# Optimization experiments

Measured on AMD Instinct MI355X. Metric: run time of the kernel, lower is better.

The kernel has to match this reference:

```python
import jax, jax.numpy as jnp
import numpy as np

H = 8  # num_heads

def layer_norm(x, g, b, eps=1e-5):
    mu = x.mean(-1, keepdims=True)
    var = ((x - mu) ** 2).mean(-1, keepdims=True)
    return (x - mu) / jnp.sqrt(var + eps) * g + b

def setup_inputs() -> dict:
    key = jax.random.key(0)
    ks = jax.random.split(key, 8)
    T, B, E, F = 64, 32, 512, 2048
    std = 0.02
    return {
        "x": jax.random.normal(ks[0], (T, B, E), jnp.float32),
        "relation": jax.random.normal(ks[1], (T, T, B, E), jnp.float32),
        "in_w": jax.random.normal(ks[2], (3 * E, E), jnp.float32) * std,
        "in_b": jnp.zeros((3 * E,), jnp.float32),
        "rel_w": jax.random.normal(ks[3], (E, 2 * E), jnp.float32) * std,
        "rel_b": jnp.zeros((2 * E,), jnp.float32),
        "out_w": jax.random.normal(ks[4], (E, E), jnp.float32) * std,
        "out_b": jnp.zeros((E,), jnp.float32),
        "fc1_w": jax.random.normal(ks[5], (E, F), jnp.float32) * std,
        "fc1_b": jnp.zeros((F,), jnp.float32),
        "fc2_w": jax.random.normal(ks[6], (F, E), jnp.float32) * std,
        "fc2_b": jnp.zeros((E,), jnp.float32),
        "ln1_g": jnp.ones((E,), jnp.float32),
        "ln1_b": jnp.zeros((E,), jnp.float32),
        "ln2_g": jnp.ones((E,), jnp.float32),
        "ln2_b": jnp.zeros((E,), jnp.float32),
    }

def reference(x, relation, in_w, in_b, rel_w, rel_b, out_w, out_b,
              fc1_w, fc1_b, fc2_w, fc2_b, ln1_g, ln1_b, ln2_g, ln2_b):
    T, B, E = x.shape
    Dh = E // H
    scaling = Dh ** -0.5
    # qkv projection (F.linear with weight [3E, E])
    qkv = x @ in_w.T + in_b                      # (T, B, 3E)
    q, k, v = jnp.split(qkv, 3, axis=-1)
    q = q.reshape(T, B * H, Dh)
    k = k.reshape(T, B * H, Dh)
    v = v.reshape(T, B * H, Dh)
    # relation bias: Conv1D(2E, E) -> ra, rb, view+transpose(0,1) as in torch
    r = relation @ rel_w + rel_b                 # (T, T, B, 2E)
    ra, rb = jnp.split(r, 2, axis=-1)
    ra = jnp.swapaxes(ra.reshape(T, T, B * H, Dh), 0, 1)
    rb = jnp.swapaxes(rb.reshape(T, T, B * H, Dh), 0, 1)
    # (q + ra) scaled, elementwise-reduce against (k + rb), extra 1/sqrt(Dh)
    q2 = (q[:, None] + ra) * scaling             # (T, T, BH, Dh)
    k2 = k[None, :] + rb                         # (T, T, BH, Dh)
    w = jnp.einsum('ijbn,ijbn->ijb', q2, k2) * scaling  # (T, T, BH)
    w = jax.nn.softmax(w, axis=1)                # softmax over src dim
    attn = jnp.einsum('ijb,jbn->bin', w, v)      # (BH, T, Dh)
    attn = jnp.swapaxes(attn, 0, 1).reshape(T, B, E)
    attn = attn @ out_w + out_b
    h = layer_norm(x + attn, ln1_g, ln1_b)
    f = jax.nn.relu(h @ fc1_w + fc1_b) @ fc2_w + fc2_b
    return layer_norm(h + f, ln2_g, ln2_b)
```

## Files before the change

kernel.cpp:

```cpp
#include <hip/hip_runtime.h>


typedef __bf16 bf16;
typedef __attribute__((ext_vector_type(8))) __bf16 bf16x8;
typedef __attribute__((ext_vector_type(4))) __bf16 bf16x4;
typedef __attribute__((ext_vector_type(4))) float f32x4;
typedef __attribute__((ext_vector_type(8))) short s16x8;


__device__ inline void fl_decode(int d, int NT, int& k, int& n) {
  int frag = d >> 9; int lane = (d >> 3) & 63; int j = d & 7;
  int kt = frag / NT, nt = frag - kt * NT;
  k = kt * 32 + ((lane >> 4) << 3) + j;
  n = nt * 16 + (lane & 15);
}

__global__ void prep_kernel(const float* __restrict__ x,
                            const float* __restrict__ in_w,
                            const float* __restrict__ rel_w,
                            const float* __restrict__ out_w,
                            const float* __restrict__ fc1_w,
                            const float* __restrict__ fc2_w,
                            bf16* __restrict__ x_b,
                            bf16* __restrict__ inw_fl,
                            bf16* __restrict__ relw_fl,
                            bf16* __restrict__ outw_fl,
                            bf16* __restrict__ fc1w_fl,
                            bf16* __restrict__ fc2w_fl) {
  int tid = blockIdx.x * 256 + threadIdx.x;
  int k, n;
  if (tid < 1048576) { x_b[tid] = (bf16)x[tid]; return; }
  tid -= 1048576;
  if (tid < 786432) {
    fl_decode(tid, 96, k, n);
    inw_fl[tid] = (bf16)in_w[n * 512 + k];
    return;
  }
  tid -= 786432;
  if (tid < 524288) {
    fl_decode(tid, 64, k, n);
    relw_fl[tid] = (bf16)rel_w[k * 1024 + n];
    return;
  }
  tid -= 524288;
  if (tid < 262144) {
    fl_decode(tid, 32, k, n);
    outw_fl[tid] = (bf16)out_w[k * 512 + n];
    return;
  }
  tid -= 262144;
  if (tid < 1048576) {
    fl_decode(tid, 128, k, n);
    fc1w_fl[tid] = (bf16)fc1_w[k * 2048 + n];
    return;
  }
  tid -= 1048576;
  if (tid < 1048576) {
    fl_decode(tid, 32, k, n);
    fc2w_fl[tid] = (bf16)fc2_w[k * 512 + n];
  }
}

template <bool RELU, bool WF32, bool WBF16>
__global__ __launch_bounds__(256, 2) void gemm_bf16(
    const bf16* __restrict__ A, const bf16* __restrict__ Bfl,
    const float* __restrict__ bias, float* __restrict__ Cf,
    bf16* __restrict__ Cb, int M, int N, int K) {
  __shared__ bf16 lA[4096];
  __shared__ bf16 lB[4096];
  const int tid = threadIdx.x;
  const int l = tid & 63;
  const int wv = tid >> 6;
  const int wm = wv >> 1, wn = wv & 1;
  const int m0 = blockIdx.x * 128, n0 = blockIdx.y * 128;
  const int NT = N >> 4;
  const int nb0 = n0 >> 4;
  const int KT = K >> 5;

  f32x4 acc[4][4];
#pragma unroll
  for (int i = 0; i < 4; i++)
#pragma unroll
    for (int j = 0; j < 4; j++) acc[i][j] = (f32x4)0.f;

  const int c = tid >> 5;
  const int lp0 = (tid & 31) * 2;

  for (int kt = 0; kt < KT; ++kt) {
#pragma unroll
    for (int u = 0; u < 2; ++u) {
      int lp = lp0 + u;
      int row = c * 16 + (lp & 15);
      int kof = (lp >> 4) << 3;
      s16x8 va = *(const s16x8*)(A + (long)(m0 + row) * K + kt * 32 + kof);
      *(s16x8*)(&lA[c * 512 + lp * 8]) = va;
    }
    {
      const s16x8* src = (const s16x8*)(Bfl + (long)(kt * NT + nb0) * 512);
      s16x8* dst = (s16x8*)lB;
      dst[tid] = src[tid];
      dst[tid + 256] = src[tid + 256];
    }
    __syncthreads();
    bf16x8 af[4], bfr[4];
#pragma unroll
    for (int mt = 0; mt < 4; mt++)
      af[mt] = *(const bf16x8*)(&lA[(wm * 4 + mt) * 512 + l * 8]);
#pragma unroll
    for (int nt = 0; nt < 4; nt++)
      bfr[nt] = *(const bf16x8*)(&lB[(wn * 4 + nt) * 512 + l * 8]);
#pragma unroll
    for (int mt = 0; mt < 4; mt++)
#pragma unroll
      for (int nt = 0; nt < 4; nt++)
        acc[mt][nt] = __builtin_amdgcn_mfma_f32_16x16x32_bf16(af[mt], bfr[nt],
                                                              acc[mt][nt], 0, 0, 0);
    __syncthreads();
  }
#pragma unroll
  for (int nt = 0; nt < 4; nt++) {
    int n = n0 + wn * 64 + nt * 16 + (l & 15);
    float bv = bias[n];
#pragma unroll
    for (int mt = 0; mt < 4; mt++) {
#pragma unroll
      for (int j = 0; j < 4; j++) {
        int row = m0 + wm * 64 + mt * 16 + ((l >> 4) << 2) + j;
        float v = acc[mt][nt][j] + bv;
        if (RELU) v = fmaxf(v, 0.f);
        if (WF32) Cf[(long)row * N + n] = v;
        if (WBF16) Cb[(long)row * N + n] = (bf16)v;
      }
    }
  }
}

__global__ __launch_bounds__(512, 2) void relw_kernel(
    const float* __restrict__ rel, const bf16* __restrict__ relw_fl,
    const float* __restrict__ rel_b, const float* __restrict__ qkv,
    float* __restrict__ wT) {
  __shared__ bf16 lA[2][2048];
  const int tid = threadIdx.x;
  const int l = tid & 63;
  const int h = tid >> 6;
  const int t1 = blockIdx.x >> 5;
  const int r2 = blockIdx.x & 31;
  const long row0 = ((long)t1 * 64 + r2 * 2) * 32;

  f32x4 acc[4][8];
#pragma unroll
  for (int i = 0; i < 4; i++)
#pragma unroll
    for (int j = 0; j < 8; j++) acc[i][j] = (f32x4)0.f;

  const int sr = tid >> 3;
  const int sg = tid & 7;
  const int smt = sr >> 4;
  const int slane = ((sg >> 1) << 4) + (sr & 15);
  const int sdst = smt * 512 + slane * 8 + (sg & 1) * 4;
  const float* srcbase = rel + (row0 + sr) * 512 + sg * 4;

  f32x4 stg = *(const f32x4*)(srcbase);
  for (int kt = 0; kt < 16; ++kt) {
    const int buf = kt & 1;
    bf16x4 cv;
#pragma unroll
    for (int u = 0; u < 4; ++u) cv[u] = (bf16)stg[u];
    *(bf16x4*)(&lA[buf][sdst]) = cv;
    f32x4 stg_next = stg;
    if (kt < 15) stg_next = *(const f32x4*)(srcbase + (kt + 1) * 32);
    __syncthreads();

    bf16x8 af[4];
#pragma unroll
    for (int mt = 0; mt < 4; mt++)
      af[mt] = *(const bf16x8*)(&lA[buf][mt * 512 + l * 8]);
    const bf16* bbase = relw_fl + ((long)kt * 64 + h * 4) * 512 + l * 8;
    bf16x8 bfr[8];
#pragma unroll
    for (int nt = 0; nt < 4; nt++) {
      bfr[nt] = *(const bf16x8*)(bbase + nt * 512);
      bfr[4 + nt] = *(const bf16x8*)(bbase + 16384 + nt * 512);
    }
#pragma unroll
    for (int mt = 0; mt < 4; mt++)
#pragma unroll
      for (int ns = 0; ns < 8; ns++)
        acc[mt][ns] = __builtin_amdgcn_mfma_f32_16x16x32_bf16(af[mt], bfr[ns],
                                                              acc[mt][ns], 0, 0, 0);
    stg = stg_next;
  }

  const int dhb = h * 64;
#pragma unroll
  for (int mt = 0; mt < 4; mt++) {
    float psum[4] = {0.f, 0.f, 0.f, 0.f};
#pragma unroll
    for (int nt = 0; nt < 4; nt++) {
      const int dh = nt * 16 + (l & 15);
      const float ba = rel_b[dhb + dh];
      const float bb2 = rel_b[512 + dhb + dh];
#pragma unroll
      for (int j = 0; j < 4; j++) {
        int rl = mt * 16 + ((l >> 4) << 2) + j;
        int b = rl & 31;
        int t2 = r2 * 2 + (rl >> 5);
        float qv = qkv[(long)(t2 * 32 + b) * 1536 + dhb + dh];
        float kv = qkv[(long)(t1 * 32 + b) * 1536 + 512 + dhb + dh];
        psum[j] += (qv + acc[mt][nt][j] + ba) * (kv + acc[mt][nt + 4][j] + bb2);
      }
    }
#pragma unroll
    for (int j = 0; j < 4; j++) {
      float v = psum[j];
      v += __shfl_xor(v, 1);
      v += __shfl_xor(v, 2);
      v += __shfl_xor(v, 4);
      v += __shfl_xor(v, 8);
      if ((l & 15) == 0) {
        int rl = mt * 16 + ((l >> 4) << 2) + j;
        int b = rl & 31;
        int i = r2 * 2 + (rl >> 5);
        wT[(long)(i * 256 + b * 8 + h) * 64 + t1] = v * 0.015625f;
      }
    }
  }
}

__global__ __launch_bounds__(256) void attn_kernel(const float* __restrict__ wT,
                                                   const float* __restrict__ qkv,
                                                   bf16* __restrict__ attn_b) {
  const int l = threadIdx.x & 63;
  const int g = blockIdx.x * 4 + (threadIdx.x >> 6);
  const int bh = g & 255;
  const int i = g >> 8;
  const int b = bh >> 3, h = bh & 7;
  float wv = wT[(long)g * 64 + l];
  float m = wv;
#pragma unroll
  for (int s = 1; s < 64; s <<= 1) m = fmaxf(m, __shfl_xor(m, s));
  float e = __expf(wv - m);
  float ssum = e;
#pragma unroll
  for (int s = 1; s < 64; s <<= 1) ssum += __shfl_xor(ssum, s);
  float p = e / ssum;
  float acc = 0.f;
  const float* vbase = qkv + 1024 + (long)b * 1536 + h * 64 + l;
#pragma unroll 8
  for (int j = 0; j < 64; ++j) {
    float pj = __shfl(p, j);
    acc = fmaf(pj, vbase[(long)j * 49152], acc);
  }
  attn_b[(long)(i * 32 + b) * 512 + h * 64 + l] = (bf16)acc;
}

template <bool WB>
__global__ __launch_bounds__(256) void ln_kernel(const float* __restrict__ a,
                                                 const float* __restrict__ res,
                                                 const float* __restrict__ g,
                                                 const float* __restrict__ bb,
                                                 float* __restrict__ of,
                                                 bf16* __restrict__ ob) {
  const int l = threadIdx.x & 63;
  const int row = blockIdx.x * 4 + (threadIdx.x >> 6);
  const float* pa = a + (long)row * 512;
  const float* pr = res + (long)row * 512;
  float xv[8];
  float s = 0.f, sq = 0.f;
#pragma unroll
  for (int u = 0; u < 8; ++u) {
    xv[u] = pa[u * 64 + l] + pr[u * 64 + l];
    s += xv[u];
    sq += xv[u] * xv[u];
  }
#pragma unroll
  for (int st = 1; st < 64; st <<= 1) {
    s += __shfl_xor(s, st);
    sq += __shfl_xor(sq, st);
  }
  float mean = s * (1.f / 512.f);
  float var = sq * (1.f / 512.f) - mean * mean;
  float rstd = rsqrtf(var + 1e-5f);
#pragma unroll
  for (int u = 0; u < 8; ++u) {
    int e = u * 64 + l;
    float v = (xv[u] - mean) * rstd * g[e] + bb[e];
    of[(long)row * 512 + e] = v;
    if (WB) ob[(long)row * 512 + e] = (bf16)v;
  }
}

extern "C" void kernel_launch(void* const* d_in, const int* in_sizes, int n_in,
                              void* d_out, int out_size, void* d_ws, size_t ws_size,
                              hipStream_t stream) {
  const float* x     = (const float*)d_in[0];
  const float* rel   = (const float*)d_in[1];
  const float* in_w  = (const float*)d_in[2];
  const float* in_b  = (const float*)d_in[3];
  const float* rel_w = (const float*)d_in[4];
  const float* rel_b = (const float*)d_in[5];
  const float* out_w = (const float*)d_in[6];
  const float* out_b = (const float*)d_in[7];
  const float* fc1_w = (const float*)d_in[8];
  const float* fc1_b = (const float*)d_in[9];
  const float* fc2_w = (const float*)d_in[10];
  const float* fc2_b = (const float*)d_in[11];
  const float* ln1_g = (const float*)d_in[12];
  const float* ln1_b = (const float*)d_in[13];
  const float* ln2_g = (const float*)d_in[14];
  const float* ln2_b = (const float*)d_in[15];

  char* ws = (char*)d_ws;
  float* qkv   = (float*)(ws + 0);
  bf16* x_b    = (bf16*)(ws + 12582912);
  bf16* inw    = (bf16*)(ws + 14680064);
  bf16* relwB  = (bf16*)(ws + 16252928);
  bf16* outwB  = (bf16*)(ws + 17301504);
  bf16* fc1wB  = (bf16*)(ws + 17825792);
  bf16* fc2wB  = (bf16*)(ws + 19922944);
  float* wT    = (float*)(ws + 22020096);
  bf16* attn   = (bf16*)(ws + 26214400);
  float* opre  = (float*)(ws + 28311552);
  float* hf    = (float*)(ws + 32505856);
  bf16* hb     = (bf16*)(ws + 36700160);
  bf16* fb     = (bf16*)(ws + 38797312);
  float* f2o   = (float*)(ws + 47185920);

  prep_kernel<<<18432, 256, 0, stream>>>(x, in_w, rel_w, out_w, fc1_w, fc2_w,
                                         x_b, inw, relwB, outwB, fc1wB, fc2wB);
  gemm_bf16<false, true, false><<<dim3(16, 12), 256, 0, stream>>>(
      x_b, inw, in_b, qkv, nullptr, 2048, 1536, 512);
  relw_kernel<<<2048, 512, 0, stream>>>(rel, relwB, rel_b, qkv, wT);
  attn_kernel<<<4096, 256, 0, stream>>>(wT, qkv, attn);
  gemm_bf16<false, true, false><<<dim3(16, 4), 256, 0, stream>>>(
      attn, outwB, out_b, opre, nullptr, 2048, 512, 512);
  ln_kernel<true><<<512, 256, 0, stream>>>(opre, x, ln1_g, ln1_b, hf, hb);
  gemm_bf16<true, false, true><<<dim3(16, 16), 256, 0, stream>>>(
      hb, fc1wB, fc1_b, nullptr, fb, 2048, 2048, 512);
  gemm_bf16<false, true, false><<<dim3(16, 4), 256, 0, stream>>>(
      fb, fc2wB, fc2_b, f2o, nullptr, 2048, 512, 2048);
  ln_kernel<false><<<512, 256, 0, stream>>>(f2o, hf, ln2_g, ln2_b, (float*)d_out,
                                            nullptr);
}
```

Before: 679.7 us.

## Vectorize weight prep, pipeline GEMMs and relation kernel, restructure attention

Weight conversion now uses vectorized float4 loads with one thread per 8 or 16 elements. The GEMM is templated on tile shape, uses direct global-to-LDS loads with double buffering, and launches smaller tiles for the narrow GEMMs so more blocks run. The relation kernel double-buffers its B-fragment register loads and prefetches activation data two steps ahead. Attention now processes one (b,h) per block, staging V and the probabilities in LDS to cut redundant strided global reads. These changes add LDS usage and register pressure, which may lower occupancy.

```diff
diff --git a/kernel.cpp b/kernel.cpp
--- a/kernel.cpp
+++ b/kernel.cpp
@@ -5,14 +5,34 @@
 typedef __attribute__((ext_vector_type(8))) __bf16 bf16x8;
 typedef __attribute__((ext_vector_type(4))) __bf16 bf16x4;
 typedef __attribute__((ext_vector_type(4))) float f32x4;
-typedef __attribute__((ext_vector_type(8))) short s16x8;
-
-
-__device__ inline void fl_decode(int d, int NT, int& k, int& n) {
-  int frag = d >> 9; int lane = (d >> 3) & 63; int j = d & 7;
+
+__device__ __forceinline__ void gl_lds16(const bf16* g, bf16* l) {
+  __builtin_amdgcn_global_load_lds((const __attribute__((address_space(1))) void*)g,
+                                   (__attribute__((address_space(3))) void*)l, 16, 0, 0);
+}
+
+__device__ __forceinline__ void block_sync_lds() {
+  asm volatile("s_waitcnt lgkmcnt(0)" ::: "memory");
+  __builtin_amdgcn_s_barrier();
+  asm volatile("" ::: "memory");
+}
+
+
+template <int NSRC, int NT>
+__device__ __forceinline__ void convkn(int t, const float* __restrict__ W,
+                                       bf16* __restrict__ dst) {
+  int frag = t >> 5, r = t & 31;
+  int lh = r >> 3, j = r & 7;
   int kt = frag / NT, nt = frag - kt * NT;
-  k = kt * 32 + ((lane >> 4) << 3) + j;
-  n = nt * 16 + (lane & 15);
+  int k = kt * 32 + lh * 8 + j;
+  const float* src = W + (long)k * NSRC + nt * 16;
+  f32x4 v0 = ((const f32x4*)src)[0], v1 = ((const f32x4*)src)[1];
+  f32x4 v2 = ((const f32x4*)src)[2], v3 = ((const f32x4*)src)[3];
+  bf16* d = dst + frag * 512 + lh * 128 + j;
+  d[0] = (bf16)v0[0];  d[8] = (bf16)v0[1];  d[16] = (bf16)v0[2];  d[24] = (bf16)v0[3];
+  d[32] = (bf16)v1[0]; d[40] = (bf16)v1[1]; d[48] = (bf16)v1[2];  d[56] = (bf16)v1[3];
+  d[64] = (bf16)v2[0]; d[72] = (bf16)v2[1]; d[80] = (bf16)v2[2];  d[88] = (bf16)v2[3];
+  d[96] = (bf16)v3[0]; d[104] = (bf16)v3[1]; d[112] = (bf16)v3[2]; d[120] = (bf16)v3[3];
 }
 
 __global__ void prep_kernel(const float* __restrict__ x,
@@ -27,105 +47,111 @@
                             bf16* __restrict__ outw_fl,
                             bf16* __restrict__ fc1w_fl,
                             bf16* __restrict__ fc2w_fl) {
-  int tid = blockIdx.x * 256 + threadIdx.x;
-  int k, n;
-  if (tid < 1048576) { x_b[tid] = (bf16)x[tid]; return; }
-  tid -= 1048576;
-  if (tid < 786432) {
-    fl_decode(tid, 96, k, n);
-    inw_fl[tid] = (bf16)in_w[n * 512 + k];
+  int t = blockIdx.x * 256 + threadIdx.x;
+  if (t < 131072) {
+    int d0 = t * 8;
+    f32x4 a = *(const f32x4*)(x + d0), b = *(const f32x4*)(x + d0 + 4);
+    bf16x8 r;
+    r[0] = (bf16)a[0]; r[1] = (bf16)a[1]; r[2] = (bf16)a[2]; r[3] = (bf16)a[3];
+    r[4] = (bf16)b[0]; r[5] = (bf16)b[1]; r[6] = (bf16)b[2]; r[7] = (bf16)b[3];
+    *(bf16x8*)(x_b + d0) = r;
     return;
   }
-  tid -= 786432;
-  if (tid < 524288) {
-    fl_decode(tid, 64, k, n);
-    relw_fl[tid] = (bf16)rel_w[k * 1024 + n];
+  t -= 131072;
+  if (t < 98304) {
+    int d0 = t * 8;
+    int frag = d0 >> 9, l = t & 63;
+    int kt = frag / 96, nt = frag - kt * 96;
+    const float* src = in_w + (long)(nt * 16 + (l & 15)) * 512 + kt * 32 + ((l >> 4) << 3);
+    f32x4 a = *(const f32x4*)src, b = *(const f32x4*)(src + 4);
+    bf16x8 r;
+    r[0] = (bf16)a[0]; r[1] = (bf16)a[1]; r[2] = (bf16)a[2]; r[3] = (bf16)a[3];
+    r[4] = (bf16)b[0]; r[5] = (bf16)b[1]; r[6] = (bf16)b[2]; r[7] = (bf16)b[3];
+    *(bf16x8*)(inw_fl + d0) = r;
     return;
   }
-  tid -= 524288;
-  if (tid < 262144) {
-    fl_decode(tid, 32, k, n);
-    outw_fl[tid] = (bf16)out_w[k * 512 + n];
-    return;
-  }
-  tid -= 262144;
-  if (tid < 1048576) {
-    fl_decode(tid, 128, k, n);
-    fc1w_fl[tid] = (bf16)fc1_w[k * 2048 + n];
-    return;
-  }
-  tid -= 1048576;
-  if (tid < 1048576) {
-    fl_decode(tid, 32, k, n);
-    fc2w_fl[tid] = (bf16)fc2_w[k * 512 + n];
-  }
-}
-
-template <bool RELU, bool WF32, bool WBF16>
+  t -= 98304;
+  if (t < 32768) { convkn<1024, 64>(t, rel_w, relw_fl); return; }
+  t -= 32768;
+  if (t < 16384) { convkn<512, 32>(t, out_w, outw_fl); return; }
+  t -= 16384;
+  if (t < 65536) { convkn<2048, 128>(t, fc1_w, fc1w_fl); return; }
+  t -= 65536;
+  if (t < 65536) { convkn<512, 32>(t, fc2_w, fc2w_fl); }
+}
+
+template <int WM, int WN, int MT, int NT, bool RELU, bool WF32, bool WBF16>
 __global__ __launch_bounds__(256, 2) void gemm_bf16(
     const bf16* __restrict__ A, const bf16* __restrict__ Bfl,
     const float* __restrict__ bias, float* __restrict__ Cf,
     bf16* __restrict__ Cb, int M, int N, int K) {
-  __shared__ bf16 lA[4096];
-  __shared__ bf16 lB[4096];
-  const int tid = threadIdx.x;
-  const int l = tid & 63;
-  const int wv = tid >> 6;
-  const int wm = wv >> 1, wn = wv & 1;
-  const int m0 = blockIdx.x * 128, n0 = blockIdx.y * 128;
-  const int NT = N >> 4;
-  const int nb0 = n0 >> 4;
-  const int KT = K >> 5;
-
-  f32x4 acc[4][4];
-#pragma unroll
-  for (int i = 0; i < 4; i++)
-#pragma unroll
-    for (int j = 0; j < 4; j++) acc[i][j] = (f32x4)0.f;
-
-  const int c = tid >> 5;
-  const int lp0 = (tid & 31) * 2;
+  constexpr int AFR = WM * MT;
+  constexpr int BFR = WN * NT;
+  constexpr int NA = AFR / 4, NB = BFR / 4;
+  __shared__ __align__(16) bf16 lA[2][AFR * 512];
+  __shared__ __align__(16) bf16 lB[2][BFR * 512];
+  const int tid = threadIdx.x, l = tid & 63, wv = tid >> 6;
+  const int wm = wv / WN, wn = wv % WN;
+  const int m0 = blockIdx.x * (AFR * 16), n0 = blockIdx.y * (BFR * 16);
+  const int NTfr = N >> 4, nb0 = n0 >> 4, KT = K >> 5;
+
+  f32x4 acc[MT][NT];
+#pragma unroll
+  for (int i = 0; i < MT; i++)
+#pragma unroll
+    for (int j = 0; j < NT; j++) acc[i][j] = (f32x4)0.f;
+
+  const bf16* pA[NA];
+#pragma unroll
+  for (int i = 0; i < NA; ++i) {
+    int f = wv + i * 4;
+    pA[i] = A + (long)(m0 + f * 16 + (l & 15)) * K + ((l >> 4) << 3);
+  }
+  const bf16* pB[NB];
+#pragma unroll
+  for (int i = 0; i < NB; ++i) {
+    int f = wv + i * 4;
+    pB[i] = Bfl + (long)(nb0 + f) * 512 + l * 8;
+  }
+#pragma unroll
+  for (int i = 0; i < NA; ++i) gl_lds16(pA[i], &lA[0][(wv + i * 4) * 512]);
+#pragma unroll
+  for (int i = 0; i < NB; ++i) gl_lds16(pB[i], &lB[0][(wv + i * 4) * 512]);
 
   for (int kt = 0; kt < KT; ++kt) {
-#pragma unroll
-    for (int u = 0; u < 2; ++u) {
-      int lp = lp0 + u;
-      int row = c * 16 + (lp & 15);
-      int kof = (lp >> 4) << 3;
-      s16x8 va = *(const s16x8*)(A + (long)(m0 + row) * K + kt * 32 + kof);
-      *(s16x8*)(&lA[c * 512 + lp * 8]) = va;
+    const int buf = kt & 1;
+    __syncthreads();
+    if (kt + 1 < KT) {
+#pragma unroll
+      for (int i = 0; i < NA; ++i)
+        gl_lds16(pA[i] + (kt + 1) * 32, &lA[buf ^ 1][(wv + i * 4) * 512]);
+#pragma unroll
+      for (int i = 0; i < NB; ++i)
+        gl_lds16(pB[i] + (long)(kt + 1) * NTfr * 512, &lB[buf ^ 1][(wv + i * 4) * 512]);
     }
-    {
-      const s16x8* src = (const s16x8*)(Bfl + (long)(kt * NT + nb0) * 512);
-      s16x8* dst = (s16x8*)lB;
-      dst[tid] = src[tid];
-      dst[tid + 256] = src[tid + 256];
-    }
-    __syncthreads();
-    bf16x8 af[4], bfr[4];
-#pragma unroll
-    for (int mt = 0; mt < 4; mt++)
-      af[mt] = *(const bf16x8*)(&lA[(wm * 4 + mt) * 512 + l * 8]);
-#pragma unroll
-    for (int nt = 0; nt < 4; nt++)
-      bfr[nt] = *(const bf16x8*)(&lB[(wn * 4 + nt) * 512 + l * 8]);
-#pragma unroll
-    for (int mt = 0; mt < 4; mt++)
-#pragma unroll
-      for (int nt = 0; nt < 4; nt++)
+    bf16x8 af[MT], bfr[NT];
+#pragma unroll
+    for (int mt = 0; mt < MT; ++mt)
+      af[mt] = *(const bf16x8*)(&lA[buf][(wm * MT + mt) * 512 + l * 8]);
+#pragma unroll
+    for (int nt = 0; nt < NT; ++nt)
+      bfr[nt] = *(const bf16x8*)(&lB[buf][(wn * NT + nt) * 512 + l * 8]);
+#pragma unroll
+    for (int mt = 0; mt < MT; ++mt)
+#pragma unroll
+      for (int nt = 0; nt < NT; ++nt)
         acc[mt][nt] = __builtin_amdgcn_mfma_f32_16x16x32_bf16(af[mt], bfr[nt],
                                                               acc[mt][nt], 0, 0, 0);
-    __syncthreads();
-  }
-#pragma unroll
-  for (int nt = 0; nt < 4; nt++) {
-    int n = n0 + wn * 64 + nt * 16 + (l & 15);
+  }
+#pragma unroll
+  for (int nt = 0; nt < NT; nt++) {
+    int n = n0 + (wn * NT + nt) * 16 + (l & 15);
     float bv = bias[n];
 #pragma unroll
-    for (int mt = 0; mt < 4; mt++) {
+    for (int mt = 0; mt < MT; mt++) {
 #pragma unroll
       for (int j = 0; j < 4; j++) {
-        int row = m0 + wm * 64 + mt * 16 + ((l >> 4) << 2) + j;
+        int row = m0 + (wm * MT + mt) * 16 + ((l >> 4) << 2) + j;
         float v = acc[mt][nt][j] + bv;
         if (RELU) v = fmaxf(v, 0.f);
         if (WF32) Cf[(long)row * N + n] = v;
@@ -135,11 +161,33 @@
   }
 }
 
+#define RELW_STEP(kt_, buf_, BC, BN, STG_W, STG_P)                               \
+  {                                                                              \
+    bf16x4 cv;                                                                   \
+    cv[0] = (bf16)STG_W[0]; cv[1] = (bf16)STG_W[1];                              \
+    cv[2] = (bf16)STG_W[2]; cv[3] = (bf16)STG_W[3];                              \
+    *(bf16x4*)(&lA[buf_][adst]) = cv;                                            \
+    block_sync_lds();                                                            \
+    if ((kt_) + 2 < 16) STG_P = *(const f32x4*)(asrc + ((kt_) + 2) * 32);        \
+    if ((kt_) + 1 < 16) {                                                        \
+      _Pragma("unroll") for (int f = 0; f < 8; ++f)                              \
+          BN[f] = *(const bf16x8*)(relw_fl + (long)((kt_) + 1) * 32768 + boff0 + \
+                                   (((f >> 2) * 32 + (f & 3)) << 9));            \
+    }                                                                            \
+    bf16x8 af[4];                                                                \
+    _Pragma("unroll") for (int mt = 0; mt < 4; mt++)                             \
+        af[mt] = *(const bf16x8*)(&lA[buf_][mt * 512 + l * 8]);                  \
+    _Pragma("unroll") for (int mt = 0; mt < 4; mt++)                             \
+        _Pragma("unroll") for (int ns = 0; ns < 8; ns++)                         \
+            acc[mt][ns] = __builtin_amdgcn_mfma_f32_16x16x32_bf16(               \
+                af[mt], BC[ns], acc[mt][ns], 0, 0, 0);                           \
+  }
+
 __global__ __launch_bounds__(512, 2) void relw_kernel(
     const float* __restrict__ rel, const bf16* __restrict__ relw_fl,
     const float* __restrict__ rel_b, const float* __restrict__ qkv,
     float* __restrict__ wT) {
-  __shared__ bf16 lA[2][2048];
+  __shared__ __align__(16) bf16 lA[2][2048];
   const int tid = threadIdx.x;
   const int l = tid & 63;
   const int h = tid >> 6;
@@ -153,42 +201,24 @@
 #pragma unroll
     for (int j = 0; j < 8; j++) acc[i][j] = (f32x4)0.f;
 
-  const int sr = tid >> 3;
-  const int sg = tid & 7;
-  const int smt = sr >> 4;
-  const int slane = ((sg >> 1) << 4) + (sr & 15);
-  const int sdst = smt * 512 + slane * 8 + (sg & 1) * 4;
-  const float* srcbase = rel + (row0 + sr) * 512 + sg * 4;
-
-  f32x4 stg = *(const f32x4*)(srcbase);
-  for (int kt = 0; kt < 16; ++kt) {
-    const int buf = kt & 1;
-    bf16x4 cv;
-#pragma unroll
-    for (int u = 0; u < 4; ++u) cv[u] = (bf16)stg[u];
-    *(bf16x4*)(&lA[buf][sdst]) = cv;
-    f32x4 stg_next = stg;
-    if (kt < 15) stg_next = *(const f32x4*)(srcbase + (kt + 1) * 32);
-    __syncthreads();
-
-    bf16x8 af[4];
-#pragma unroll
-    for (int mt = 0; mt < 4; mt++)
-      af[mt] = *(const bf16x8*)(&lA[buf][mt * 512 + l * 8]);
-    const bf16* bbase = relw_fl + ((long)kt * 64 + h * 4) * 512 + l * 8;
-    bf16x8 bfr[8];
-#pragma unroll
-    for (int nt = 0; nt < 4; nt++) {
-      bfr[nt] = *(const bf16x8*)(bbase + nt * 512);
-      bfr[4 + nt] = *(const bf16x8*)(bbase + 16384 + nt * 512);
-    }
-#pragma unroll
-    for (int mt = 0; mt < 4; mt++)
-#pragma unroll
-      for (int ns = 0; ns < 8; ns++)
-        acc[mt][ns] = __builtin_amdgcn_mfma_f32_16x16x32_bf16(af[mt], bfr[ns],
-                                                              acc[mt][ns], 0, 0, 0);
-    stg = stg_next;
+  const int slot = tid >> 1, half = tid & 1;
+  const int fA = slot >> 6, l2 = slot & 63;
+  const float* asrc =
+      rel + (row0 + fA * 16 + (l2 & 15)) * 512 + ((l2 >> 4) << 3) + half * 4;
+  const int adst = fA * 512 + l2 * 8 + half * 4;
+
+  const int boff0 = h * 2048 + l * 8;
+
+  f32x4 stgA = *(const f32x4*)asrc;
+  f32x4 stgB = *(const f32x4*)(asrc + 32);
+  bf16x8 b0[8], b1[8];
+#pragma unroll
+  for (int f = 0; f < 8; ++f)
+    b0[f] = *(const bf16x8*)(relw_fl + boff0 + (((f >> 2) * 32 + (f & 3)) << 9));
+
+  for (int kt = 0; kt < 16; kt += 2) {
+    RELW_STEP(kt, 0, b0, b1, stgA, stgA)
+    RELW_STEP(kt + 1, 1, b1, b0, stgB, stgB)
   }
 
   const int dhb = h * 64;
@@ -230,28 +260,72 @@
 __global__ __launch_bounds__(256) void attn_kernel(const float* __restrict__ wT,
                                                    const float* __restrict__ qkv,
                                                    bf16* __restrict__ attn_b) {
-  const int l = threadIdx.x & 63;
-  const int g = blockIdx.x * 4 + (threadIdx.x >> 6);
-  const int bh = g & 255;
-  const int i = g >> 8;
-  const int b = bh >> 3, h = bh & 7;
-  float wv = wT[(long)g * 64 + l];
-  float m = wv;
-#pragma unroll
-  for (int s = 1; s < 64; s <<= 1) m = fmaxf(m, __shfl_xor(m, s));
-  float e = __expf(wv - m);
-  float ssum = e;
-#pragma unroll
-  for (int s = 1; s < 64; s <<= 1) ssum += __shfl_xor(ssum, s);
-  float p = e / ssum;
-  float acc = 0.f;
-  const float* vbase = qkv + 1024 + (long)b * 1536 + h * 64 + l;
-#pragma unroll 8
+  __shared__ __align__(16) float s[64][68];
+  __shared__ __align__(16) float vl[64][68];
+  __shared__ float pm[64][4], ps[64][4];
+  const int tid = threadIdx.x;
+  const int b = blockIdx.x >> 3, h = blockIdx.x & 7;
+  const int i = tid >> 2, g = tid & 3;
+
+  const float* wsrc = wT + ((long)i * 256 + b * 8 + h) * 64 + g * 16;
+  f32x4 w0 = ((const f32x4*)wsrc)[0], w1 = ((const f32x4*)wsrc)[1];
+  f32x4 w2 = ((const f32x4*)wsrc)[2], w3 = ((const f32x4*)wsrc)[3];
+  const float* vsrc = qkv + ((long)i * 32 + b) * 1536 + 1024 + h * 64 + g * 16;
+  f32x4 v0 = ((const f32x4*)vsrc)[0], v1 = ((const f32x4*)vsrc)[1];
+  f32x4 v2 = ((const f32x4*)vsrc)[2], v3 = ((const f32x4*)vsrc)[3];
+  *(f32x4*)&vl[i][g * 16] = v0;
+  *(f32x4*)&vl[i][g * 16 + 4] = v1;
+  *(f32x4*)&vl[i][g * 16 + 8] = v2;
+  *(f32x4*)&vl[i][g * 16 + 12] = v3;
+  float pmax = -1e30f;
+#pragma unroll
+  for (int u = 0; u < 4; ++u) {
+    pmax = fmaxf(pmax, fmaxf(fmaxf(w0[u], w1[u]), fmaxf(w2[u], w3[u])));
+  }
+  pm[i][g] = pmax;
+  __syncthreads();
+  float m = fmaxf(fmaxf(pm[i][0], pm[i][1]), fmaxf(pm[i][2], pm[i][3]));
+  float psum = 0.f;
+  f32x4 e0, e1, e2, e3;
+#pragma unroll
+  for (int u = 0; u < 4; ++u) {
+    e0[u] = __expf(w0[u] - m); psum += e0[u];
+    e1[u] = __expf(w1[u] - m); psum += e1[u];
+    e2[u] = __expf(w2[u] - m); psum += e2[u];
+    e3[u] = __expf(w3[u] - m); psum += e3[u];
+  }
+  *(f32x4*)&s[i][g * 16] = e0;
+  *(f32x4*)&s[i][g * 16 + 4] = e1;
+  *(f32x4*)&s[i][g * 16 + 8] = e2;
+  *(f32x4*)&s[i][g * 16 + 12] = e3;
+  ps[i][g] = psum;
+  __syncthreads();
+  float scale = 1.f / (ps[i][0] + ps[i][1] + ps[i][2] + ps[i][3]);
+  f32x4 o0 = (f32x4)0.f, o1 = (f32x4)0.f, o2 = (f32x4)0.f, o3 = (f32x4)0.f;
   for (int j = 0; j < 64; ++j) {
-    float pj = __shfl(p, j);
-    acc = fmaf(pj, vbase[(long)j * 49152], acc);
-  }
-  attn_b[(long)(i * 32 + b) * 512 + h * 64 + l] = (bf16)acc;
+    float pj = s[i][j];
+    const float* vr = &vl[j][g * 16];
+    f32x4 a0 = ((const f32x4*)vr)[0], a1 = ((const f32x4*)vr)[1];
+    f32x4 a2 = ((const f32x4*)vr)[2], a3 = ((const f32x4*)vr)[3];
+#pragma unroll
+    for (int u = 0; u < 4; ++u) {
+      o0[u] = fmaf(pj, a0[u], o0[u]);
+      o1[u] = fmaf(pj, a1[u], o1[u]);
+      o2[u] = fmaf(pj, a2[u], o2[u]);
+      o3[u] = fmaf(pj, a3[u], o3[u]);
+    }
+  }
+  bf16x8 r0, r1;
+#pragma unroll
+  for (int u = 0; u < 4; ++u) {
+    r0[u] = (bf16)(o0[u] * scale);
+    r0[4 + u] = (bf16)(o1[u] * scale);
+    r1[u] = (bf16)(o2[u] * scale);
+    r1[4 + u] = (bf16)(o3[u] * scale);
+  }
+  bf16* dst = attn_b + ((long)i * 32 + b) * 512 + h * 64 + g * 16;
+  *(bf16x8*)dst = r0;
+  *(bf16x8*)(dst + 8) = r1;
 }
 
 template <bool WB>
@@ -326,18 +400,18 @@
   bf16* fb     = (bf16*)(ws + 38797312);
   float* f2o   = (float*)(ws + 47185920);
 
-  prep_kernel<<<18432, 256, 0, stream>>>(x, in_w, rel_w, out_w, fc1_w, fc2_w,
-                                         x_b, inw, relwB, outwB, fc1wB, fc2wB);
-  gemm_bf16<false, true, false><<<dim3(16, 12), 256, 0, stream>>>(
+  prep_kernel<<<1600, 256, 0, stream>>>(x, in_w, rel_w, out_w, fc1_w, fc2_w,
+                                        x_b, inw, relwB, outwB, fc1wB, fc2wB);
+  gemm_bf16<2, 2, 2, 4, false, true, false><<<dim3(32, 12), 256, 0, stream>>>(
       x_b, inw, in_b, qkv, nullptr, 2048, 1536, 512);
   relw_kernel<<<2048, 512, 0, stream>>>(rel, relwB, rel_b, qkv, wT);
-  attn_kernel<<<4096, 256, 0, stream>>>(wT, qkv, attn);
-  gemm_bf16<false, true, false><<<dim3(16, 4), 256, 0, stream>>>(
+  attn_kernel<<<256, 256, 0, stream>>>(wT, qkv, attn);
+  gemm_bf16<2, 2, 2, 2, false, true, false><<<dim3(32, 8), 256, 0, stream>>>(
       attn, outwB, out_b, opre, nullptr, 2048, 512, 512);
   ln_kernel<true><<<512, 256, 0, stream>>>(opre, x, ln1_g, ln1_b, hf, hb);
-  gemm_bf16<true, false, true><<<dim3(16, 16), 256, 0, stream>>>(
+  gemm_bf16<2, 2, 4, 4, true, false, true><<<dim3(16, 16), 256, 0, stream>>>(
       hb, fc1wB, fc1_b, nullptr, fb, 2048, 2048, 512);
-  gemm_bf16<false, true, false><<<dim3(16, 4), 256, 0, stream>>>(
+  gemm_bf16<2, 2, 2, 2, false, true, false><<<dim3(32, 8), 256, 0, stream>>>(
       fb, fc2wB, fc2_b, f2o, nullptr, 2048, 512, 2048);
   ln_kernel<false><<<512, 256, 0, stream>>>(f2o, hf, ln2_g, ln2_b, (float*)d_out,
                                             nullptr);
```

Result: faster. 648.9 us (-4.5%).
